# Kernel tuning notes

Measured on AMD Instinct MI355X. Metric: run time of the kernel, lower is better.

Reference implementation:

```python
import jax, jax.numpy as jnp
import numpy as np

DIM = 512
NUM_HEADS = 1
WS = 16
B, H, W = 2, WS * WS, 1


def _rel_pos_index(ws):
    # matches Attention.calculate_relative_position_index (no Swin offset -> negatives)
    coords = np.stack(np.meshgrid(np.arange(ws), np.arange(ws), indexing='ij'), 0).reshape(2, -1)
    rel = coords[:, :, None] - coords[:, None, :]          # [2, ws^2, ws^2]
    return rel.transpose(1, 2, 0).sum(-1)                  # [ws^2, ws^2] in [-(2ws-2), 2ws-2]

_NTAB = (2 * WS - 1) ** 2
# torch fancy indexing wraps negative indices; emulate with mod (values are in (-NTAB, NTAB))
_RPI = np.mod(_rel_pos_index(WS), _NTAB).reshape(-1)       # [ws^4]


def setup_inputs() -> dict:
    key = jax.random.key(0)
    ks = jax.random.split(key, 6)
    x = jax.random.normal(ks[0], (B, DIM, H, W), dtype=jnp.float32)
    qkv_w = jax.random.normal(ks[1], (3 * DIM, DIM), dtype=jnp.float32) * (DIM ** -0.5)
    qkv_b = jax.random.normal(ks[2], (3 * DIM,), dtype=jnp.float32) * 0.02
    proj_w = jax.random.normal(ks[3], (DIM, DIM), dtype=jnp.float32) * (DIM ** -0.5)
    proj_b = jax.random.normal(ks[4], (DIM,), dtype=jnp.float32) * 0.02
    rpb = jax.random.normal(ks[5], (_NTAB, NUM_HEADS), dtype=jnp.float32) * 0.02
    return {"x": x, "qkv_w": qkv_w, "qkv_b": qkv_b,
            "proj_w": proj_w, "proj_b": proj_b, "rpb": rpb}


def reference(x, qkv_w, qkv_b, proj_w, proj_b, rpb):
    b, c, h, w = x.shape                                   # [B, C, H, W=1]
    d = c // NUM_HEADS
    scale = d ** -0.5                                      # qk_scale=None -> (dim//nh)^-0.5
    # 1x1 conv == channel matmul
    qkv = jnp.einsum('bchw,oc->bohw', x, qkv_w) + qkv_b[None, :, None, None]
    qkv = qkv.reshape(b, 3, NUM_HEADS, d, h, w)
    q, k, v = qkv[:, 0], qkv[:, 1], qkv[:, 2]              # [B, nh, d, H, W]
    # matmul over last two dims: contracts W -> [B, nh, d, H, H]
    attn = jnp.einsum('bndhw,bndgw->bndhg', q, k) * scale
    idx = jnp.asarray(_RPI)
    bias = rpb[idx].reshape(h * w, h * w, -1).transpose(2, 0, 1)  # [nh, HW, HW] = [1, H, H]
    attn = jax.nn.softmax(attn + bias, axis=-1)
    out = jnp.einsum('bndhg,bndgw->bndhw', attn, v).sum(axis=1)   # sum over heads -> [B, d, H, W]
    out = jnp.einsum('bchw,oc->bohw', out, proj_w) + proj_b[None, :, None, None]
    return out
```

## Files before the change

### kernel.cpp

```cpp
#include <hip/hip_runtime.h>
#include <hip/hip_bf16.h>


#define TOK   256
#define KDIM  512
#define LOG2E 1.4426950408889634f
#define SCALE 0.04419417382415922f

#define EXP2(x) __builtin_amdgcn_exp2f(x)

template<int KSPLIT>
__global__ __launch_bounds__(256)
void gemm_f32(const float* __restrict__ A, const float* __restrict__ B,
              float* __restrict__ C, int M)
{
    constexpr int KLEN = KDIM / KSPLIT;
    const int t  = threadIdx.x;
    const int ty = t >> 4;
    const int tx = t & 15;
    const int o0 = blockIdx.x * 64;
    const int h0 = blockIdx.y * 64;
    const int b  = blockIdx.z / KSPLIT;
    const int ks = blockIdx.z % KSPLIT;

    const float* Ab = A + (size_t)o0 * KDIM + ks * KLEN;
    const float* Bb = B + ((size_t)b * KDIM + (size_t)ks * KLEN) * TOK + h0;
    float*       Cb = C + (((size_t)(ks * 2 + b) * M) + o0) * TOK + h0;

    __shared__ float As[16][64];
    __shared__ float Bs[16][64];

    const int ar  = t >> 2;
    const int ac4 = (t & 3) * 4;
    const int bk  = t >> 4;
    const int bh4 = (t & 15) * 4;

    float acc[4][4];
#pragma unroll
    for (int i = 0; i < 4; ++i)
#pragma unroll
        for (int j = 0; j < 4; ++j) acc[i][j] = 0.f;

    for (int k0 = 0; k0 < KLEN; k0 += 16) {
        const float4 av = *(const float4*)(Ab + (size_t)ar * KDIM + (k0 + ac4));
        const float4 bv = *(const float4*)(Bb + (size_t)(k0 + bk) * TOK + bh4);
        __syncthreads();
        As[ac4 + 0][ar] = av.x;
        As[ac4 + 1][ar] = av.y;
        As[ac4 + 2][ar] = av.z;
        As[ac4 + 3][ar] = av.w;
        *(float4*)&Bs[bk][bh4] = bv;
        __syncthreads();
#pragma unroll
        for (int kk = 0; kk < 16; ++kk) {
            const float4 a4 = *(const float4*)&As[kk][ty * 4];
            const float4 b4 = *(const float4*)&Bs[kk][tx * 4];
            const float a[4] = {a4.x, a4.y, a4.z, a4.w};
            const float bb[4] = {b4.x, b4.y, b4.z, b4.w};
#pragma unroll
            for (int i = 0; i < 4; ++i)
#pragma unroll
                for (int j = 0; j < 4; ++j)
                    acc[i][j] = fmaf(a[i], bb[j], acc[i][j]);
        }
    }

#pragma unroll
    for (int i = 0; i < 4; ++i) {
        const float4 o4 = make_float4(acc[i][0], acc[i][1], acc[i][2], acc[i][3]);
        *(float4*)(Cb + (size_t)(ty * 4 + i) * TOK + tx * 4) = o4;
    }
}

__global__ __launch_bounds__(256)
void attn_f32(const float* __restrict__ qkvp, const float* __restrict__ qkv_b,
              const float* __restrict__ rpb, float* __restrict__ aout)
{
    __shared__ float ks_[2][TOK];
    __shared__ float vs_[2][TOK];
    __shared__ float tab2[64];
    __shared__ float brow[31][258];
    __shared__ float lpart[2][TOK];
    __shared__ float apart[2][TOK];

    const int t  = threadIdx.x;
    const int b  = blockIdx.y;
    const int d0 = blockIdx.x * 2;
    const float* q0 = qkvp + (size_t)b * (1536 * TOK);
    const size_t P1 = (size_t)786432;

    if (t < 61) {
        const int rel = t - 30;
        tab2[t] = rpb[rel < 0 ? rel + 961 : rel] * LOG2E;
    }
    {
        const int sel = t >> 7;
        const int row = (t >> 6) & 1;
        const int g4  = (t & 63) * 4;
        const int o   = (sel ? 1024 : 512) + d0 + row;
        const float* p = q0 + (size_t)o * TOK + g4;
        const float4 x0 = *(const float4*)p;
        const float4 x1 = *(const float4*)(p + P1);
        const float bb = qkv_b[o];
        float4 v;
        v.x = x0.x + x1.x + bb;
        v.y = x0.y + x1.y + bb;
        v.z = x0.z + x1.z + bb;
        v.w = x0.w + x1.w + bb;
        if (sel == 0) {
            const float s = SCALE * LOG2E;
            v.x *= s; v.y *= s; v.z *= s; v.w *= s;
            *(float4*)&ks_[row][g4] = v;
        } else {
            *(float4*)&vs_[row][g4] = v;
        }
    }
    __syncthreads();
    {
        const int rg = ((t >> 4) & 15) + (t & 15);
#pragma unroll 1
        for (int it = 0; it < 31; ++it)
            brow[it][t] = tab2[it - rg + 30];
    }
    __syncthreads();

    const int w   = t >> 6;
    const int dl  = w & 1;
    const int gh  = w >> 1;
    const int hl  = t & 63;
    const int qi  = ((hl & 15) << 2) | (hl >> 4);
    const int h0  = qi * 4;
    const int rh0 = (qi >> 2) + 4 * (qi & 3);

    float q[4];
    {
        const float* p = q0 + (size_t)(d0 + dl) * TOK + h0;
        const float4 x0 = *(const float4*)p;
        const float4 x1 = *(const float4*)(p + P1);
        const float bb = qkv_b[d0 + dl];
        q[0] = x0.x + x1.x + bb;
        q[1] = x0.y + x1.y + bb;
        q[2] = x0.z + x1.z + bb;
        q[3] = x0.w + x1.w + bb;
    }

    float l[4]  = {0.f, 0.f, 0.f, 0.f};
    float am[4] = {0.f, 0.f, 0.f, 0.f};

    const int pbeg = gh * 128;
#pragma unroll 2
    for (int p = pbeg; p < pbeg + 128; p += 4) {
        const float4 k4 = *(const float4*)&ks_[dl][p];
        const float4 v4 = *(const float4*)&vs_[dl][p];
#pragma unroll
        for (int r = 0; r < 4; ++r) {
            const float2 b01 = *(const float2*)&brow[rh0 + r][p];
            const float2 b23 = *(const float2*)&brow[rh0 + r][p + 2];
            float e;
            e = EXP2(fmaf(q[r], k4.x, b01.x)); l[r] += e; am[r] = fmaf(e, v4.x, am[r]);
            e = EXP2(fmaf(q[r], k4.y, b01.y)); l[r] += e; am[r] = fmaf(e, v4.y, am[r]);
            e = EXP2(fmaf(q[r], k4.z, b23.x)); l[r] += e; am[r] = fmaf(e, v4.z, am[r]);
            e = EXP2(fmaf(q[r], k4.w, b23.y)); l[r] += e; am[r] = fmaf(e, v4.w, am[r]);
        }
    }

    if (gh == 1) {
        *(float4*)&lpart[dl][h0] = make_float4(l[0], l[1], l[2], l[3]);
        *(float4*)&apart[dl][h0] = make_float4(am[0], am[1], am[2], am[3]);
    }
    __syncthreads();
    if (gh == 0) {
        const float4 lo = *(const float4*)&lpart[dl][h0];
        const float4 ao = *(const float4*)&apart[dl][h0];
        float4 o4;
        o4.x = (am[0] + ao.x) / (l[0] + lo.x);
        o4.y = (am[1] + ao.y) / (l[1] + lo.y);
        o4.z = (am[2] + ao.z) / (l[2] + lo.z);
        o4.w = (am[3] + ao.w) / (l[3] + lo.w);
        *(float4*)(aout + ((size_t)b * 512 + d0 + dl) * TOK + h0) = o4;
    }
}

__global__ __launch_bounds__(256)
void combine_f32(const float* __restrict__ pp, const float* __restrict__ pb,
                 float* __restrict__ out)
{
    const int gid  = blockIdx.x * 256 + threadIdx.x;
    const int flat = gid * 4;
    const int o = (flat >> 8) & 511;
    float4 a        = *(const float4*)(pp + flat);
    const float4 b4 = *(const float4*)(pp + 262144 + flat);
    const float4 c4 = *(const float4*)(pp + 524288 + flat);
    const float4 d4 = *(const float4*)(pp + 786432 + flat);
    const float bias = pb[o];
    a.x += b4.x + c4.x + d4.x + bias;
    a.y += b4.y + c4.y + d4.y + bias;
    a.z += b4.z + c4.z + d4.z + bias;
    a.w += b4.w + c4.w + d4.w + bias;
    *(float4*)(out + flat) = a;
}

extern "C" void kernel_launch(void* const* d_in, const int* in_sizes, int n_in,
                              void* d_out, int out_size, void* d_ws, size_t ws_size,
                              hipStream_t stream)
{
    const float* x      = (const float*)d_in[0];
    const float* qkv_w  = (const float*)d_in[1];
    const float* qkv_b  = (const float*)d_in[2];
    const float* proj_w = (const float*)d_in[3];
    const float* proj_b = (const float*)d_in[4];
    const float* rpb    = (const float*)d_in[5];
    float* out = (float*)d_out;
    float* ws  = (float*)d_ws;

    float* qkvp  = ws;
    float* aout  = ws + 1572864;
    float* projp = ws + 1835008;

    gemm_f32<2><<<dim3(24, 4, 4), 256, 0, stream>>>(qkv_w, x, qkvp, 1536);

    attn_f32<<<dim3(256, 2), 256, 0, stream>>>(qkvp, qkv_b, rpb, aout);

    gemm_f32<4><<<dim3(8, 4, 8), 256, 0, stream>>>(proj_w, aout, projp, 512);

    combine_f32<<<dim3(256), 256, 0, stream>>>(projp, proj_b, out);
}
```

Baseline: 108.6 us.

## Double-buffer GEMM tiles, widen QKV tile to 128 rows, split K eight ways

The FP32 GEMM now double-buffers its shared-memory tiles with register prefetch, which removes one barrier per k-step. The QKV GEMM uses 128-row tiles with an 8x4 per-thread micro-tile and a padded A stride. Both GEMMs split K into eight parts, so the attention and combine kernels now reduce eight partial buffers instead of two or four. This buys more blocks and better overlap of loads with math, but costs much larger workspace traffic for the partial sums: 8x1536x256x2 floats for QKV, read again by every attention block.

Result: faster. 103.3 us (-4.8%).

```diff
diff --git a/kernel.cpp b/kernel.cpp
--- a/kernel.cpp
+++ b/kernel.cpp
@@ -6,70 +6,109 @@
 #define KDIM  512
 #define LOG2E 1.4426950408889634f
 #define SCALE 0.04419417382415922f
+#define NPART 8
+#define QPSTRIDE 786432
+#define PPSTRIDE 262144
 
 #define EXP2(x) __builtin_amdgcn_exp2f(x)
 
-template<int KSPLIT>
+template<int BM, int KSPLIT>
 __global__ __launch_bounds__(256)
 void gemm_f32(const float* __restrict__ A, const float* __restrict__ B,
               float* __restrict__ C, int M)
 {
-    constexpr int KLEN = KDIM / KSPLIT;
+    constexpr int KLEN  = KDIM / KSPLIT;
+    constexpr int NITER = KLEN / 16;
+    constexpr int MM    = BM / 16;
+    constexpr int LDA   = BM + 4;
+
+    __shared__ float As[2][16][LDA];
+    __shared__ float Bs[2][16][64];
+
     const int t  = threadIdx.x;
-    const int ty = t >> 4;
-    const int tx = t & 15;
-    const int o0 = blockIdx.x * 64;
-    const int h0 = blockIdx.y * 64;
-    const int b  = blockIdx.z / KSPLIT;
-    const int ks = blockIdx.z % KSPLIT;
+    const int o0 = blockIdx.x * BM;
+    const int n0 = blockIdx.y * 64;
+    const int b  = blockIdx.z & 1;
+    const int ks = blockIdx.z >> 1;
 
     const float* Ab = A + (size_t)o0 * KDIM + ks * KLEN;
-    const float* Bb = B + ((size_t)b * KDIM + (size_t)ks * KLEN) * TOK + h0;
-    float*       Cb = C + (((size_t)(ks * 2 + b) * M) + o0) * TOK + h0;
-
-    __shared__ float As[16][64];
-    __shared__ float Bs[16][64];
+    const float* Bb = B + ((size_t)b * KDIM + (size_t)ks * KLEN) * TOK + n0;
+    float*       Cb = C + ((size_t)blockIdx.z * M + o0) * TOK + n0;
 
     const int ar  = t >> 2;
     const int ac4 = (t & 3) * 4;
     const int bk  = t >> 4;
-    const int bh4 = (t & 15) * 4;
-
-    float acc[4][4];
-#pragma unroll
-    for (int i = 0; i < 4; ++i)
+    const int bn4 = (t & 15) * 4;
+
+    float4 ra0, ra1, rb;
+#define LOAD_TILE(IT) do {                                                   \
+        const int k0_ = (IT) * 16;                                           \
+        ra0 = *(const float4*)(Ab + (size_t)ar * KDIM + k0_ + ac4);          \
+        if (BM == 128)                                                       \
+            ra1 = *(const float4*)(Ab + (size_t)(64 + ar) * KDIM + k0_ + ac4);\
+        rb  = *(const float4*)(Bb + (size_t)(k0_ + bk) * TOK + bn4);         \
+    } while (0)
+#define STORE_TILE(BUF) do {                                                 \
+        As[BUF][ac4 + 0][ar] = ra0.x;                                        \
+        As[BUF][ac4 + 1][ar] = ra0.y;                                        \
+        As[BUF][ac4 + 2][ar] = ra0.z;                                        \
+        As[BUF][ac4 + 3][ar] = ra0.w;                                        \
+        if (BM == 128) {                                                     \
+            As[BUF][ac4 + 0][64 + ar] = ra1.x;                               \
+            As[BUF][ac4 + 1][64 + ar] = ra1.y;                               \
+            As[BUF][ac4 + 2][64 + ar] = ra1.z;                               \
+            As[BUF][ac4 + 3][64 + ar] = ra1.w;                               \
+        }                                                                    \
+        *(float4*)&Bs[BUF][bk][bn4] = rb;                                    \
+    } while (0)
+
+    const int m0 = (t >> 4) * MM;
+    const int n4 = (t & 15) * 4;
+
+    float acc[MM][4];
+#pragma unroll
+    for (int i = 0; i < MM; ++i)
 #pragma unroll
         for (int j = 0; j < 4; ++j) acc[i][j] = 0.f;
 
-    for (int k0 = 0; k0 < KLEN; k0 += 16) {
-        const float4 av = *(const float4*)(Ab + (size_t)ar * KDIM + (k0 + ac4));
-        const float4 bv = *(const float4*)(Bb + (size_t)(k0 + bk) * TOK + bh4);
+    LOAD_TILE(0);
+    STORE_TILE(0);
+    if (NITER > 1) LOAD_TILE(1);
+    __syncthreads();
+
+#pragma unroll
+    for (int it = 0; it < NITER; ++it) {
+        const int cur = it & 1;
+        if (it + 1 < NITER) STORE_TILE(1 - cur);
+        if (it + 2 < NITER) LOAD_TILE(it + 2);
+#pragma unroll
+        for (int kk = 0; kk < 16; ++kk) {
+            const float4 b4 = *(const float4*)&Bs[cur][kk][n4];
+            float af[MM];
+#pragma unroll
+            for (int mi = 0; mi < MM; mi += 4) {
+                const float4 a4 = *(const float4*)&As[cur][kk][m0 + mi];
+                af[mi + 0] = a4.x; af[mi + 1] = a4.y;
+                af[mi + 2] = a4.z; af[mi + 3] = a4.w;
+            }
+#pragma unroll
+            for (int mi = 0; mi < MM; ++mi) {
+                acc[mi][0] = fmaf(af[mi], b4.x, acc[mi][0]);
+                acc[mi][1] = fmaf(af[mi], b4.y, acc[mi][1]);
+                acc[mi][2] = fmaf(af[mi], b4.z, acc[mi][2]);
+                acc[mi][3] = fmaf(af[mi], b4.w, acc[mi][3]);
+            }
+        }
         __syncthreads();
-        As[ac4 + 0][ar] = av.x;
-        As[ac4 + 1][ar] = av.y;
-        As[ac4 + 2][ar] = av.z;
-        As[ac4 + 3][ar] = av.w;
-        *(float4*)&Bs[bk][bh4] = bv;
-        __syncthreads();
-#pragma unroll
-        for (int kk = 0; kk < 16; ++kk) {
-            const float4 a4 = *(const float4*)&As[kk][ty * 4];
-            const float4 b4 = *(const float4*)&Bs[kk][tx * 4];
-            const float a[4] = {a4.x, a4.y, a4.z, a4.w};
-            const float bb[4] = {b4.x, b4.y, b4.z, b4.w};
-#pragma unroll
-            for (int i = 0; i < 4; ++i)
-#pragma unroll
-                for (int j = 0; j < 4; ++j)
-                    acc[i][j] = fmaf(a[i], bb[j], acc[i][j]);
-        }
-    }
-
-#pragma unroll
-    for (int i = 0; i < 4; ++i) {
-        const float4 o4 = make_float4(acc[i][0], acc[i][1], acc[i][2], acc[i][3]);
-        *(float4*)(Cb + (size_t)(ty * 4 + i) * TOK + tx * 4) = o4;
-    }
+    }
+
+#pragma unroll
+    for (int mi = 0; mi < MM; ++mi) {
+        const float4 o4 = make_float4(acc[mi][0], acc[mi][1], acc[mi][2], acc[mi][3]);
+        *(float4*)(Cb + (size_t)(m0 + mi) * TOK + n4) = o4;
+    }
+#undef LOAD_TILE
+#undef STORE_TILE
 }
 
 __global__ __launch_bounds__(256)
@@ -87,7 +126,6 @@
     const int b  = blockIdx.y;
     const int d0 = blockIdx.x * 2;
     const float* q0 = qkvp + (size_t)b * (1536 * TOK);
-    const size_t P1 = (size_t)786432;
 
     if (t < 61) {
         const int rel = t - 30;
@@ -99,14 +137,13 @@
         const int g4  = (t & 63) * 4;
         const int o   = (sel ? 1024 : 512) + d0 + row;
         const float* p = q0 + (size_t)o * TOK + g4;
-        const float4 x0 = *(const float4*)p;
-        const float4 x1 = *(const float4*)(p + P1);
         const float bb = qkv_b[o];
-        float4 v;
-        v.x = x0.x + x1.x + bb;
-        v.y = x0.y + x1.y + bb;
-        v.z = x0.z + x1.z + bb;
-        v.w = x0.w + x1.w + bb;
+        float4 v = make_float4(bb, bb, bb, bb);
+#pragma unroll
+        for (int pp = 0; pp < NPART; ++pp) {
+            const float4 x = *(const float4*)(p + (size_t)pp * QPSTRIDE);
+            v.x += x.x; v.y += x.y; v.z += x.z; v.w += x.w;
+        }
         if (sel == 0) {
             const float s = SCALE * LOG2E;
             v.x *= s; v.y *= s; v.z *= s; v.w *= s;
@@ -135,13 +172,13 @@
     float q[4];
     {
         const float* p = q0 + (size_t)(d0 + dl) * TOK + h0;
-        const float4 x0 = *(const float4*)p;
-        const float4 x1 = *(const float4*)(p + P1);
         const float bb = qkv_b[d0 + dl];
-        q[0] = x0.x + x1.x + bb;
-        q[1] = x0.y + x1.y + bb;
-        q[2] = x0.z + x1.z + bb;
-        q[3] = x0.w + x1.w + bb;
+        q[0] = bb; q[1] = bb; q[2] = bb; q[3] = bb;
+#pragma unroll
+        for (int pp = 0; pp < NPART; ++pp) {
+            const float4 x = *(const float4*)(p + (size_t)pp * QPSTRIDE);
+            q[0] += x.x; q[1] += x.y; q[2] += x.z; q[3] += x.w;
+        }
     }
 
     float l[4]  = {0.f, 0.f, 0.f, 0.f};
@@ -188,15 +225,12 @@
     const int gid  = blockIdx.x * 256 + threadIdx.x;
     const int flat = gid * 4;
     const int o = (flat >> 8) & 511;
-    float4 a        = *(const float4*)(pp + flat);
-    const float4 b4 = *(const float4*)(pp + 262144 + flat);
-    const float4 c4 = *(const float4*)(pp + 524288 + flat);
-    const float4 d4 = *(const float4*)(pp + 786432 + flat);
-    const float bias = pb[o];
-    a.x += b4.x + c4.x + d4.x + bias;
-    a.y += b4.y + c4.y + d4.y + bias;
-    a.z += b4.z + c4.z + d4.z + bias;
-    a.w += b4.w + c4.w + d4.w + bias;
+    float4 a = make_float4(pb[o], pb[o], pb[o], pb[o]);
+#pragma unroll
+    for (int p = 0; p < NPART; ++p) {
+        const float4 x = *(const float4*)(pp + (size_t)p * PPSTRIDE + flat);
+        a.x += x.x; a.y += x.y; a.z += x.z; a.w += x.w;
+    }
     *(float4*)(out + flat) = a;
 }
 
@@ -214,14 +248,14 @@
     float* ws  = (float*)d_ws;
 
     float* qkvp  = ws;
-    float* aout  = ws + 1572864;
-    float* projp = ws + 1835008;
-
-    gemm_f32<2><<<dim3(24, 4, 4), 256, 0, stream>>>(qkv_w, x, qkvp, 1536);
+    float* aout  = ws + 6291456;
+    float* projp = ws + 6553600;
+
+    gemm_f32<128, 8><<<dim3(12, 4, 16), 256, 0, stream>>>(qkv_w, x, qkvp, 1536);
 
     attn_f32<<<dim3(256, 2), 256, 0, stream>>>(qkvp, qkv_b, rpb, aout);
 
-    gemm_f32<4><<<dim3(8, 4, 8), 256, 0, stream>>>(proj_w, aout, projp, 512);
+    gemm_f32<64, 8><<<dim3(8, 4, 16), 256, 0, stream>>>(proj_w, aout, projp, 512);
 
     combine_f32<<<dim3(256), 256, 0, stream>>>(projp, proj_b, out);
 }
```

## Fuse QKV projection into attention kernel and fold split-K reduction into projection

Applied to the files above, without the earlier changes.

Drops the separate tiled QKV GEMM. Each attention block now computes its own six q/k/v channel rows directly from x, reducing the partial sums across four waves in shared memory, and reuses a union for the reduction buffer and the bias table. The output projection becomes a single kernel that reduces split-K in shared memory and adds the bias, removing the combine kernel and the partial-sum round trips. This cuts four launches to two and avoids intermediate global traffic. In exchange, x is re-read by every attention block and the GEMMs lose register tiling, relying on scalar weight loads and L2 reuse.

Result: no change. 110.4 us (+1.6%).

```diff
diff --git a/kernel.cpp b/kernel.cpp
--- a/kernel.cpp
+++ b/kernel.cpp
@@ -9,153 +9,122 @@
 
 #define EXP2(x) __builtin_amdgcn_exp2f(x)
 
-template<int KSPLIT>
+struct K1Smem {
+    union {
+        float red[4][6][256];
+        float brow[31][258];
+    } u;
+    float tab2[64];
+    float ks_[2][TOK];
+    float vs_[2][TOK];
+    float qs_[2][TOK];
+    float lpart[2][TOK], apart[2][TOK];
+};
+
 __global__ __launch_bounds__(256)
-void gemm_f32(const float* __restrict__ A, const float* __restrict__ B,
-              float* __restrict__ C, int M)
+void qkv_attn(const float* __restrict__ x, const float* __restrict__ qkv_w,
+              const float* __restrict__ qkv_b, const float* __restrict__ rpb,
+              float* __restrict__ aout)
 {
-    constexpr int KLEN = KDIM / KSPLIT;
-    const int t  = threadIdx.x;
-    const int ty = t >> 4;
-    const int tx = t & 15;
-    const int o0 = blockIdx.x * 64;
-    const int h0 = blockIdx.y * 64;
-    const int b  = blockIdx.z / KSPLIT;
-    const int ks = blockIdx.z % KSPLIT;
-
-    const float* Ab = A + (size_t)o0 * KDIM + ks * KLEN;
-    const float* Bb = B + ((size_t)b * KDIM + (size_t)ks * KLEN) * TOK + h0;
-    float*       Cb = C + (((size_t)(ks * 2 + b) * M) + o0) * TOK + h0;
-
-    __shared__ float As[16][64];
-    __shared__ float Bs[16][64];
-
-    const int ar  = t >> 2;
-    const int ac4 = (t & 3) * 4;
-    const int bk  = t >> 4;
-    const int bh4 = (t & 15) * 4;
-
-    float acc[4][4];
-#pragma unroll
-    for (int i = 0; i < 4; ++i)
-#pragma unroll
-        for (int j = 0; j < 4; ++j) acc[i][j] = 0.f;
-
-    for (int k0 = 0; k0 < KLEN; k0 += 16) {
-        const float4 av = *(const float4*)(Ab + (size_t)ar * KDIM + (k0 + ac4));
-        const float4 bv = *(const float4*)(Bb + (size_t)(k0 + bk) * TOK + bh4);
-        __syncthreads();
-        As[ac4 + 0][ar] = av.x;
-        As[ac4 + 1][ar] = av.y;
-        As[ac4 + 2][ar] = av.z;
-        As[ac4 + 3][ar] = av.w;
-        *(float4*)&Bs[bk][bh4] = bv;
-        __syncthreads();
-#pragma unroll
-        for (int kk = 0; kk < 16; ++kk) {
-            const float4 a4 = *(const float4*)&As[kk][ty * 4];
-            const float4 b4 = *(const float4*)&Bs[kk][tx * 4];
-            const float a[4] = {a4.x, a4.y, a4.z, a4.w};
-            const float bb[4] = {b4.x, b4.y, b4.z, b4.w};
-#pragma unroll
-            for (int i = 0; i < 4; ++i)
-#pragma unroll
-                for (int j = 0; j < 4; ++j)
-                    acc[i][j] = fmaf(a[i], bb[j], acc[i][j]);
-        }
-    }
-
-#pragma unroll
-    for (int i = 0; i < 4; ++i) {
-        const float4 o4 = make_float4(acc[i][0], acc[i][1], acc[i][2], acc[i][3]);
-        *(float4*)(Cb + (size_t)(ty * 4 + i) * TOK + tx * 4) = o4;
-    }
-}
-
-__global__ __launch_bounds__(256)
-void attn_f32(const float* __restrict__ qkvp, const float* __restrict__ qkv_b,
-              const float* __restrict__ rpb, float* __restrict__ aout)
-{
-    __shared__ float ks_[2][TOK];
-    __shared__ float vs_[2][TOK];
-    __shared__ float tab2[64];
-    __shared__ float brow[31][258];
-    __shared__ float lpart[2][TOK];
-    __shared__ float apart[2][TOK];
-
-    const int t  = threadIdx.x;
-    const int b  = blockIdx.y;
-    const int d0 = blockIdx.x * 2;
-    const float* q0 = qkvp + (size_t)b * (1536 * TOK);
-    const size_t P1 = (size_t)786432;
+    __shared__ K1Smem sm;
+    const int t    = threadIdx.x;
+    const int d0   = blockIdx.x * 2;
+    const int b    = blockIdx.y;
+    const int w    = t >> 6;
+    const int lane = t & 63;
 
     if (t < 61) {
         const int rel = t - 30;
-        tab2[t] = rpb[rel < 0 ? rel + 961 : rel] * LOG2E;
-    }
-    {
-        const int sel = t >> 7;
-        const int row = (t >> 6) & 1;
-        const int g4  = (t & 63) * 4;
-        const int o   = (sel ? 1024 : 512) + d0 + row;
-        const float* p = q0 + (size_t)o * TOK + g4;
-        const float4 x0 = *(const float4*)p;
-        const float4 x1 = *(const float4*)(p + P1);
-        const float bb = qkv_b[o];
-        float4 v;
-        v.x = x0.x + x1.x + bb;
-        v.y = x0.y + x1.y + bb;
-        v.z = x0.z + x1.z + bb;
-        v.w = x0.w + x1.w + bb;
-        if (sel == 0) {
-            const float s = SCALE * LOG2E;
-            v.x *= s; v.y *= s; v.z *= s; v.w *= s;
-            *(float4*)&ks_[row][g4] = v;
-        } else {
-            *(float4*)&vs_[row][g4] = v;
-        }
-    }
-    __syncthreads();
+        sm.tab2[t] = rpb[rel < 0 ? rel + 961 : rel] * LOG2E;
+    }
+
+    {
+        const float* xb = x + (size_t)b * (KDIM * TOK);
+        const int g0 = lane * 4;
+        const float* wp[6];
+        wp[0] = qkv_w + (size_t)(d0 + 0) * KDIM;
+        wp[1] = qkv_w + (size_t)(d0 + 1) * KDIM;
+        wp[2] = qkv_w + (size_t)(512 + d0 + 0) * KDIM;
+        wp[3] = qkv_w + (size_t)(512 + d0 + 1) * KDIM;
+        wp[4] = qkv_w + (size_t)(1024 + d0 + 0) * KDIM;
+        wp[5] = qkv_w + (size_t)(1024 + d0 + 1) * KDIM;
+
+        float acc[6][4];
+#pragma unroll
+        for (int e = 0; e < 6; ++e)
+#pragma unroll
+            for (int j = 0; j < 4; ++j) acc[e][j] = 0.f;
+
+        const int cbeg = w * 128;
+#pragma unroll 1
+        for (int c = cbeg; c < cbeg + 128; c += 4) {
+            float4 xv[4];
+#pragma unroll
+            for (int u = 0; u < 4; ++u)
+                xv[u] = *(const float4*)(xb + (size_t)(c + u) * TOK + g0);
+#pragma unroll
+            for (int u = 0; u < 4; ++u) {
+#pragma unroll
+                for (int e = 0; e < 6; ++e) {
+                    const float wv = wp[e][c + u];
+                    acc[e][0] = fmaf(wv, xv[u].x, acc[e][0]);
+                    acc[e][1] = fmaf(wv, xv[u].y, acc[e][1]);
+                    acc[e][2] = fmaf(wv, xv[u].z, acc[e][2]);
+                    acc[e][3] = fmaf(wv, xv[u].w, acc[e][3]);
+                }
+            }
+        }
+#pragma unroll
+        for (int e = 0; e < 6; ++e)
+            *(float4*)&sm.u.red[w][e][g0] = make_float4(acc[e][0], acc[e][1],
+                                                        acc[e][2], acc[e][3]);
+    }
+    __syncthreads();
+
+    {
+#pragma unroll
+        for (int e = 0; e < 6; ++e) {
+            const float v = sm.u.red[0][e][t] + sm.u.red[1][e][t] +
+                            sm.u.red[2][e][t] + sm.u.red[3][e][t];
+            if (e < 2)      sm.qs_[e][t] = v + qkv_b[d0 + e];
+            else if (e < 4) sm.ks_[e - 2][t] = (v + qkv_b[512 + d0 + e - 2]) *
+                                               (SCALE * LOG2E);
+            else            sm.vs_[e - 4][t] = v + qkv_b[1024 + d0 + e - 4];
+        }
+    }
+    __syncthreads();
+
     {
         const int rg = ((t >> 4) & 15) + (t & 15);
 #pragma unroll 1
         for (int it = 0; it < 31; ++it)
-            brow[it][t] = tab2[it - rg + 30];
-    }
-    __syncthreads();
-
-    const int w   = t >> 6;
+            sm.u.brow[it][t] = sm.tab2[it - rg + 30];
+    }
+    __syncthreads();
+
     const int dl  = w & 1;
     const int gh  = w >> 1;
-    const int hl  = t & 63;
-    const int qi  = ((hl & 15) << 2) | (hl >> 4);
+    const int qi  = ((lane & 15) << 2) | (lane >> 4);
     const int h0  = qi * 4;
     const int rh0 = (qi >> 2) + 4 * (qi & 3);
 
     float q[4];
     {
-        const float* p = q0 + (size_t)(d0 + dl) * TOK + h0;
-        const float4 x0 = *(const float4*)p;
-        const float4 x1 = *(const float4*)(p + P1);
-        const float bb = qkv_b[d0 + dl];
-        q[0] = x0.x + x1.x + bb;
-        q[1] = x0.y + x1.y + bb;
-        q[2] = x0.z + x1.z + bb;
-        q[3] = x0.w + x1.w + bb;
+        const float4 q4 = *(const float4*)&sm.qs_[dl][h0];
+        q[0] = q4.x; q[1] = q4.y; q[2] = q4.z; q[3] = q4.w;
     }
 
     float l[4]  = {0.f, 0.f, 0.f, 0.f};
     float am[4] = {0.f, 0.f, 0.f, 0.f};
-
     const int pbeg = gh * 128;
 #pragma unroll 2
     for (int p = pbeg; p < pbeg + 128; p += 4) {
-        const float4 k4 = *(const float4*)&ks_[dl][p];
-        const float4 v4 = *(const float4*)&vs_[dl][p];
+        const float4 k4 = *(const float4*)&sm.ks_[dl][p];
+        const float4 v4 = *(const float4*)&sm.vs_[dl][p];
 #pragma unroll
         for (int r = 0; r < 4; ++r) {
-            const float2 b01 = *(const float2*)&brow[rh0 + r][p];
-            const float2 b23 = *(const float2*)&brow[rh0 + r][p + 2];
+            const float2 b01 = *(const float2*)&sm.u.brow[rh0 + r][p];
+            const float2 b23 = *(const float2*)&sm.u.brow[rh0 + r][p + 2];
             float e;
             e = EXP2(fmaf(q[r], k4.x, b01.x)); l[r] += e; am[r] = fmaf(e, v4.x, am[r]);
             e = EXP2(fmaf(q[r], k4.y, b01.y)); l[r] += e; am[r] = fmaf(e, v4.y, am[r]);
@@ -165,13 +134,13 @@
     }
 
     if (gh == 1) {
-        *(float4*)&lpart[dl][h0] = make_float4(l[0], l[1], l[2], l[3]);
-        *(float4*)&apart[dl][h0] = make_float4(am[0], am[1], am[2], am[3]);
+        *(float4*)&sm.lpart[dl][h0] = make_float4(l[0], l[1], l[2], l[3]);
+        *(float4*)&sm.apart[dl][h0] = make_float4(am[0], am[1], am[2], am[3]);
     }
     __syncthreads();
     if (gh == 0) {
-        const float4 lo = *(const float4*)&lpart[dl][h0];
-        const float4 ao = *(const float4*)&apart[dl][h0];
+        const float4 lo = *(const float4*)&sm.lpart[dl][h0];
+        const float4 ao = *(const float4*)&sm.apart[dl][h0];
         float4 o4;
         o4.x = (am[0] + ao.x) / (l[0] + lo.x);
         o4.y = (am[1] + ao.y) / (l[1] + lo.y);
@@ -182,22 +151,59 @@
 }
 
 __global__ __launch_bounds__(256)
-void combine_f32(const float* __restrict__ pp, const float* __restrict__ pb,
-                 float* __restrict__ out)
+void proj_fused(const float* __restrict__ aout, const float* __restrict__ proj_w,
+                const float* __restrict__ proj_b, float* __restrict__ out)
 {
-    const int gid  = blockIdx.x * 256 + threadIdx.x;
-    const int flat = gid * 4;
-    const int o = (flat >> 8) & 511;
-    float4 a        = *(const float4*)(pp + flat);
-    const float4 b4 = *(const float4*)(pp + 262144 + flat);
-    const float4 c4 = *(const float4*)(pp + 524288 + flat);
-    const float4 d4 = *(const float4*)(pp + 786432 + flat);
-    const float bias = pb[o];
-    a.x += b4.x + c4.x + d4.x + bias;
-    a.y += b4.y + c4.y + d4.y + bias;
-    a.z += b4.z + c4.z + d4.z + bias;
-    a.w += b4.w + c4.w + d4.w + bias;
-    *(float4*)(out + flat) = a;
+    __shared__ float sred[4][4][256];
+    const int t    = threadIdx.x;
+    const int o0   = blockIdx.x * 4;
+    const int b    = blockIdx.y;
+    const int w    = t >> 6;
+    const int g0   = (t & 63) * 4;
+
+    const float* ab = aout + (size_t)b * (KDIM * TOK);
+    const float* wp[4];
+#pragma unroll
+    for (int e = 0; e < 4; ++e)
+        wp[e] = proj_w + (size_t)(o0 + e) * KDIM;
+
+    float acc[4][4];
+#pragma unroll
+    for (int e = 0; e < 4; ++e)
+#pragma unroll
+        for (int j = 0; j < 4; ++j) acc[e][j] = 0.f;
+
+    const int cbeg = w * 128;
+#pragma unroll 1
+    for (int c = cbeg; c < cbeg + 128; c += 4) {
+        float4 av[4];
+#pragma unroll
+        for (int u = 0; u < 4; ++u)
+            av[u] = *(const float4*)(ab + (size_t)(c + u) * TOK + g0);
+#pragma unroll
+        for (int u = 0; u < 4; ++u) {
+#pragma unroll
+            for (int e = 0; e < 4; ++e) {
+                const float wv = wp[e][c + u];
+                acc[e][0] = fmaf(wv, av[u].x, acc[e][0]);
+                acc[e][1] = fmaf(wv, av[u].y, acc[e][1]);
+                acc[e][2] = fmaf(wv, av[u].z, acc[e][2]);
+                acc[e][3] = fmaf(wv, av[u].w, acc[e][3]);
+            }
+        }
+    }
+#pragma unroll
+    for (int e = 0; e < 4; ++e)
+        *(float4*)&sred[w][e][g0] = make_float4(acc[e][0], acc[e][1],
+                                                acc[e][2], acc[e][3]);
+    __syncthreads();
+
+#pragma unroll
+    for (int e = 0; e < 4; ++e) {
+        const float v = sred[0][e][t] + sred[1][e][t] +
+                        sred[2][e][t] + sred[3][e][t] + proj_b[o0 + e];
+        out[((size_t)b * 512 + o0 + e) * TOK + t] = v;
+    }
 }
 
 extern "C" void kernel_launch(void* const* d_in, const int* in_sizes, int n_in,
@@ -210,18 +216,10 @@
     const float* proj_w = (const float*)d_in[3];
     const float* proj_b = (const float*)d_in[4];
     const float* rpb    = (const float*)d_in[5];
-    float* out = (float*)d_out;
-    float* ws  = (float*)d_ws;
-
-    float* qkvp  = ws;
-    float* aout  = ws + 1572864;
-    float* projp = ws + 1835008;
-
-    gemm_f32<2><<<dim3(24, 4, 4), 256, 0, stream>>>(qkv_w, x, qkvp, 1536);
-
-    attn_f32<<<dim3(256, 2), 256, 0, stream>>>(qkvp, qkv_b, rpb, aout);
-
-    gemm_f32<4><<<dim3(8, 4, 8), 256, 0, stream>>>(proj_w, aout, projp, 512);
-
-    combine_f32<<<dim3(256), 256, 0, stream>>>(projp, proj_b, out);
+    float* out  = (float*)d_out;
+    float* aout = (float*)d_ws;
+
+    qkv_attn<<<dim3(256, 2), 256, 0, stream>>>(x, qkv_w, qkv_b, rpb, aout);
+
+    proj_fused<<<dim3(128, 2), 256, 0, stream>>>(aout, proj_w, proj_b, out);
 }
```
